# Optimization experiments

Measured on AMD Instinct MI355X. Metric: run time of the kernel, lower is better.

Reference implementation:

```python
import jax, jax.numpy as jnp
import numpy as np

B, S, D, H = 2, 2048, 1024, 16
DK = D // H

def setup_inputs() -> dict:
    key = jax.random.key(0)
    ks = jax.random.split(key, 8)
    inp = {
        "Q": jax.random.normal(ks[0], (B, S, D), dtype=jnp.float32),
        "K": jax.random.normal(ks[1], (B, S, D), dtype=jnp.float32),
        "V": jax.random.normal(ks[2], (B, S, D), dtype=jnp.float32),
        "mask": jax.random.randint(ks[3], (B, 1, S, S), 0, 2, dtype=jnp.int32),
        # nn.Linear weights, shape [out_features, in_features], no bias
        "Wq": jax.random.normal(ks[4], (D, D), dtype=jnp.float32) / np.sqrt(D),
        "Wk": jax.random.normal(ks[5], (D, D), dtype=jnp.float32) / np.sqrt(D),
        "Wv": jax.random.normal(ks[6], (D, D), dtype=jnp.float32) / np.sqrt(D),
        "Wo": jax.random.normal(ks[7], (D, D), dtype=jnp.float32) / np.sqrt(D),
    }
    return inp

def reference(Q, K, V, mask, Wq, Wk, Wv, Wo):
    b, s, d = Q.shape
    # projections: y = x @ W.T (torch nn.Linear convention)
    q = (Q @ Wq.T).reshape(b, s, H, DK).transpose(0, 2, 1, 3)  # [b,h,s,dk]
    k = (K @ Wk.T).reshape(b, -1, H, DK).transpose(0, 2, 1, 3)
    v = (V @ Wv.T).reshape(b, -1, H, DK).transpose(0, 2, 1, 3)
    score = jnp.einsum("bhqd,bhkd->bhqk", q, k) / jnp.sqrt(jnp.float32(DK))
    # faithful to source: masked positions get value 1e-9 BEFORE softmax
    score = jnp.where(mask == 0, jnp.float32(1e-9), score)
    attn = jax.nn.softmax(score, axis=-1)
    # dropout p=0.1 treated as eval-mode identity
    out = jnp.einsum("bhqk,bhkd->bhqd", attn, v)  # [b,h,s,dk]
    out = out.transpose(0, 2, 1, 3).reshape(b, s, d)
    return out @ Wo.T
```

## Files before the change

kernel.cpp:

```cpp
#include <hip/hip_runtime.h>

typedef unsigned short u16;
typedef __attribute__((ext_vector_type(8))) short bf16x8;
typedef __attribute__((ext_vector_type(4))) float f32x4;

constexpr int B_  = 2;
constexpr int S_  = 2048;
constexpr int D_  = 1024;
constexpr int H_  = 16;
constexpr int DK_ = 64;
constexpr int NROW = B_ * S_;
constexpr size_t QSZ  = (size_t)B_ * H_ * S_ * DK_;
constexpr size_t XBSZ = (size_t)NROW * D_;
constexpr size_t WBSZ = (size_t)D_ * D_;

__device__ __forceinline__ u16 f2bf(float f) {
    union { float f; unsigned u; } c; c.f = f;
    unsigned r = c.u + 0x7fffu + ((c.u >> 16) & 1u);
    return (u16)(r >> 16);
}
__device__ __forceinline__ unsigned pack2(float a, float b) {
    return (unsigned)f2bf(a) | ((unsigned)f2bf(b) << 16);
}

__device__ __forceinline__ void gl_lds16(const u16* g, u16* l) {
    __builtin_amdgcn_global_load_lds(
        (const __attribute__((address_space(1))) void*)g,
        (__attribute__((address_space(3))) void*)l, 16, 0, 0);
}

__global__ __launch_bounds__(256)
void cvt7(const float* __restrict__ s0, const float* __restrict__ s1,
          const float* __restrict__ s2, const float* __restrict__ s3,
          const float* __restrict__ s4, const float* __restrict__ s5,
          const float* __restrict__ s6,
          u16* __restrict__ d0, u16* __restrict__ d1, u16* __restrict__ d2,
          u16* __restrict__ d3, u16* __restrict__ d4, u16* __restrict__ d5,
          u16* __restrict__ d6)
{
    constexpr size_t XT = 3 * XBSZ;
    constexpr int NCHUNK = (int)((3 * XBSZ + 4 * WBSZ) / 2048);

    for (int c = blockIdx.x; c < NCHUNK; c += gridDim.x) {
        const size_t base = (size_t)c * 2048;
        const float* s; u16* d; size_t off;
        if (base < XT) {
            const int a = (int)(base >> 22);
            off = base & (XBSZ - 1);
            s = (a == 0) ? s0 : (a == 1) ? s1 : s2;
            d = (a == 0) ? d0 : (a == 1) ? d1 : d2;
        } else {
            const size_t r = base - XT;
            const int a = (int)(r >> 20);
            off = r & (WBSZ - 1);
            s = (a == 0) ? s3 : (a == 1) ? s4 : (a == 2) ? s5 : s6;
            d = (a == 0) ? d3 : (a == 1) ? d4 : (a == 2) ? d5 : d6;
        }
        const size_t e = off + (size_t)threadIdx.x * 8;
        const float4 x0 = *(const float4*)(s + e);
        const float4 x1 = *(const float4*)(s + e + 4);
        uint4 p;
        p.x = pack2(x0.x, x0.y); p.y = pack2(x0.z, x0.w);
        p.z = pack2(x1.x, x1.y); p.w = pack2(x1.z, x1.w);
        *(uint4*)(d + e) = p;
    }
}

__global__ __launch_bounds__(256, 3)
void qkv_gemm(const u16* __restrict__ Xq, const u16* __restrict__ Xk,
              const u16* __restrict__ Xv,
              const u16* __restrict__ Wq, const u16* __restrict__ Wk,
              const u16* __restrict__ Wv,
              u16* __restrict__ Yq, u16* __restrict__ Yk, u16* __restrict__ Yv)
{
    __shared__ u16 As[128 * 32];
    __shared__ u16 Bs[128 * 32];

    const int z = blockIdx.z;
    const u16* X = (z == 0) ? Xq : (z == 1) ? Xk : Xv;
    const u16* W = (z == 0) ? Wq : (z == 1) ? Wk : Wv;
    u16*       Y = (z == 0) ? Yq : (z == 1) ? Yk : Yv;
    const float osc = (z == 0) ? 0.125f : 1.0f;

    const int tid  = threadIdx.x;
    const int lane = tid & 63;
    const int w    = tid >> 6;
    const int quad = lane >> 4;
    const int lq   = lane & 15;
    const int wm   = (w & 1) << 6;
    const int wn   = (w >> 1) << 6;

    const int m0 = blockIdx.x << 7;
    const int n0 = blockIdx.y << 7;

    const int srow = tid >> 2;
    const int scol = (tid & 3) << 3;
    const u16* ga0 = X + (size_t)(m0 + srow) * D_ + scol;
    const u16* ga1 = ga0 + (size_t)64 * D_;
    const u16* gb0 = W + (size_t)(n0 + srow) * D_ + scol;
    const u16* gb1 = gb0 + (size_t)64 * D_;

    u16* la0 = As + (size_t)w * 512;
    u16* la1 = As + 2048 + (size_t)w * 512;
    u16* lb0 = Bs + (size_t)w * 512;
    u16* lb1 = Bs + 2048 + (size_t)w * 512;

    f32x4 acc[4][4];
#pragma unroll
    for (int i = 0; i < 4; ++i)
#pragma unroll
        for (int j = 0; j < 4; ++j) acc[i][j] = (f32x4){0.f, 0.f, 0.f, 0.f};

    for (int kt = 0; kt < D_; kt += 32) {
        __syncthreads();
        gl_lds16(ga0 + kt, la0);
        gl_lds16(ga1 + kt, la1);
        gl_lds16(gb0 + kt, lb0);
        gl_lds16(gb1 + kt, lb1);
        __syncthreads();

        bf16x8 af[4], bf[4];
#pragma unroll
        for (int t = 0; t < 4; ++t) {
            af[t] = *(const bf16x8*)&As[(size_t)(wm + (t << 4) + lq) * 32 + (quad << 3)];
            bf[t] = *(const bf16x8*)&Bs[(size_t)(wn + (t << 4) + lq) * 32 + (quad << 3)];
        }
#pragma unroll
        for (int i = 0; i < 4; ++i)
#pragma unroll
            for (int j = 0; j < 4; ++j)
                acc[i][j] = __builtin_amdgcn_mfma_f32_16x16x32_bf16(
                    af[i], bf[j], acc[i][j], 0, 0, 0);
    }

#pragma unroll
    for (int i = 0; i < 4; ++i)
#pragma unroll
        for (int j = 0; j < 4; ++j)
#pragma unroll
            for (int r = 0; r < 4; ++r) {
                const int grow = m0 + wm + (i << 4) + (quad << 2) + r;
                const int of   = n0 + wn + (j << 4) + lq;
                const int b = grow >> 11, s = grow & (S_ - 1);
                const int h = of >> 6,    dk = of & 63;
                Y[(((size_t)(b * H_ + h)) * S_ + s) * DK_ + dk] =
                    f2bf(acc[i][j][r] * osc);
            }
}

__global__ __launch_bounds__(256, 3)
void out_gemm(const u16* __restrict__ X, const u16* __restrict__ W,
              float* __restrict__ Y)
{
    __shared__ u16 As[128 * 32];
    __shared__ u16 Bs[128 * 32];

    const int tid  = threadIdx.x;
    const int lane = tid & 63;
    const int w    = tid >> 6;
    const int quad = lane >> 4;
    const int lq   = lane & 15;
    const int wm   = (w & 1) << 6;
    const int wn   = (w >> 1) << 6;

    const int m0 = blockIdx.x << 7;
    const int n0 = blockIdx.y << 7;

    const int srow = tid >> 2;
    const int scol = (tid & 3) << 3;
    const u16* ga0 = X + (size_t)(m0 + srow) * D_ + scol;
    const u16* ga1 = ga0 + (size_t)64 * D_;
    const u16* gb0 = W + (size_t)(n0 + srow) * D_ + scol;
    const u16* gb1 = gb0 + (size_t)64 * D_;

    u16* la0 = As + (size_t)w * 512;
    u16* la1 = As + 2048 + (size_t)w * 512;
    u16* lb0 = Bs + (size_t)w * 512;
    u16* lb1 = Bs + 2048 + (size_t)w * 512;

    f32x4 acc[4][4];
#pragma unroll
    for (int i = 0; i < 4; ++i)
#pragma unroll
        for (int j = 0; j < 4; ++j) acc[i][j] = (f32x4){0.f, 0.f, 0.f, 0.f};

    for (int kt = 0; kt < D_; kt += 32) {
        __syncthreads();
        gl_lds16(ga0 + kt, la0);
        gl_lds16(ga1 + kt, la1);
        gl_lds16(gb0 + kt, lb0);
        gl_lds16(gb1 + kt, lb1);
        __syncthreads();

        bf16x8 af[4], bf[4];
#pragma unroll
        for (int t = 0; t < 4; ++t) {
            af[t] = *(const bf16x8*)&As[(size_t)(wm + (t << 4) + lq) * 32 + (quad << 3)];
            bf[t] = *(const bf16x8*)&Bs[(size_t)(wn + (t << 4) + lq) * 32 + (quad << 3)];
        }
#pragma unroll
        for (int i = 0; i < 4; ++i)
#pragma unroll
            for (int j = 0; j < 4; ++j)
                acc[i][j] = __builtin_amdgcn_mfma_f32_16x16x32_bf16(
                    af[i], bf[j], acc[i][j], 0, 0, 0);
    }

#pragma unroll
    for (int i = 0; i < 4; ++i)
#pragma unroll
        for (int j = 0; j < 4; ++j)
#pragma unroll
            for (int r = 0; r < 4; ++r) {
                const int grow = m0 + wm + (i << 4) + (quad << 2) + r;
                const int gcol = n0 + wn + (j << 4) + lq;
                Y[(size_t)grow * D_ + gcol] = acc[i][j][r];
            }
}

constexpr int AP = 72;

__global__ __launch_bounds__(256, 2)
void attn_mfma4(const u16* __restrict__ qb, const u16* __restrict__ kb,
                const u16* __restrict__ vb, const int* __restrict__ mask,
                u16* __restrict__ ctx)
{
    __shared__ u16 Qs[128][AP];
    __shared__ u16 Ks[64][AP];
    __shared__ u16 Vt[64][AP];
    __shared__ u16 Ps[128][AP];

    const int tid  = threadIdx.x;
    const int lane = tid & 63;
    const int w    = tid >> 6;
    const int quad = lane >> 4;
    const int lq   = lane & 15;
    const int w32  = w << 5;

    const int q0 = blockIdx.x << 7;
    const int h  = blockIdx.y;
    const int b  = blockIdx.z;

    const u16* qbh = qb + (((size_t)b * H_ + h) * S_ + q0) * DK_;
    const u16* kbh = kb + ((size_t)b * H_ + h) * S_ * DK_;
    const u16* vbh = vb + ((size_t)b * H_ + h) * S_ * DK_;
    const int* mbh = mask + (size_t)b * S_ * S_;

    {
        const int r = tid >> 1, c = (tid & 1) << 5;
#pragma unroll
        for (int u = 0; u < 4; ++u)
            *(uint4*)&Qs[r][c + (u << 3)] =
                *(const uint4*)&qbh[(size_t)r * DK_ + c + (u << 3)];
    }
    __syncthreads();
    bf16x8 aQ[2][2];
#pragma unroll
    for (int i = 0; i < 2; ++i) {
        aQ[i][0] = *(const bf16x8*)&Qs[w32 + (i << 4) + lq][quad << 3];
        aQ[i][1] = *(const bf16x8*)&Qs[w32 + (i << 4) + lq][32 + (quad << 3)];
    }

    f32x4 O[2][4];
    float lsum[2][4];
#pragma unroll
    for (int i = 0; i < 2; ++i)
#pragma unroll
        for (int t = 0; t < 4; ++t) O[i][t] = (f32x4){0.f, 0.f, 0.f, 0.f};
#pragma unroll
    for (int i = 0; i < 2; ++i)
#pragma unroll
        for (int r = 0; r < 4; ++r) lsum[i][r] = 0.f;

    const int ksr = tid >> 2, ksc = (tid & 3) << 4;
    const int vkey = lane, vsc = w << 4;
    const int vpc  = ((vkey & 15) << 2) | (vkey >> 4);

    uint4 kr0, kr1; ushort4 vr[4];
    {
        kr0 = *(const uint4*)&kbh[(size_t)ksr * DK_ + ksc];
        kr1 = *(const uint4*)&kbh[(size_t)ksr * DK_ + ksc + 8];
#pragma unroll
        for (int u = 0; u < 4; ++u)
            vr[u] = *(const ushort4*)&vbh[(size_t)vkey * DK_ + vsc + (u << 2)];
    }

    const int qrow0 = q0 + w32 + (quad << 2);

    for (int k0 = 0; k0 < S_; k0 += 64) {
        int mreg[2][4][4];
#pragma unroll
        for (int i = 0; i < 2; ++i)
#pragma unroll
            for (int r = 0; r < 4; ++r)
#pragma unroll
                for (int t = 0; t < 4; ++t)
                    mreg[i][r][t] =
                        mbh[(size_t)(qrow0 + (i << 4) + r) * S_ + k0 + (t << 4) + lq];

        __syncthreads();
        {
            *(uint4*)&Ks[ksr][ksc]     = kr0;
            *(uint4*)&Ks[ksr][ksc + 8] = kr1;
            const u16 vv[16] = {
                vr[0].x, vr[0].y, vr[0].z, vr[0].w,
                vr[1].x, vr[1].y, vr[1].z, vr[1].w,
                vr[2].x, vr[2].y, vr[2].z, vr[2].w,
                vr[3].x, vr[3].y, vr[3].z, vr[3].w };
#pragma unroll
            for (int i = 0; i < 16; ++i)
                Vt[vsc + i][vpc] = vv[i];
        }
        __syncthreads();

        if (k0 + 64 < S_) {
            const size_t kb0 = (size_t)(k0 + 64 + ksr) * DK_ + ksc;
            kr0 = *(const uint4*)&kbh[kb0];
            kr1 = *(const uint4*)&kbh[kb0 + 8];
            const size_t vb0 = (size_t)(k0 + 64 + vkey) * DK_ + vsc;
#pragma unroll
            for (int u = 0; u < 4; ++u)
                vr[u] = *(const ushort4*)&vbh[vb0 + (u << 2)];
        }

        f32x4 st[2][4];
#pragma unroll
        for (int t = 0; t < 4; ++t) {
            const bf16x8 b0 = *(const bf16x8*)&Ks[(t << 4) + lq][quad << 3];
            const bf16x8 b1 = *(const bf16x8*)&Ks[(t << 4) + lq][32 + (quad << 3)];
#pragma unroll
            for (int i = 0; i < 2; ++i) {
                f32x4 c = {0.f, 0.f, 0.f, 0.f};
                c = __builtin_amdgcn_mfma_f32_16x16x32_bf16(aQ[i][0], b0, c, 0, 0, 0);
                c = __builtin_amdgcn_mfma_f32_16x16x32_bf16(aQ[i][1], b1, c, 0, 0, 0);
                st[i][t] = c;
            }
        }

#pragma unroll
        for (int i = 0; i < 2; ++i)
#pragma unroll
            for (int r = 0; r < 4; ++r) {
                float p0 = __expf(st[i][0][r]);
                float p1 = __expf(st[i][1][r]);
                float p2 = __expf(st[i][2][r]);
                float p3 = __expf(st[i][3][r]);
                p0 = (mreg[i][r][0] == 0) ? 1.0f : p0;
                p1 = (mreg[i][r][1] == 0) ? 1.0f : p1;
                p2 = (mreg[i][r][2] == 0) ? 1.0f : p2;
                p3 = (mreg[i][r][3] == 0) ? 1.0f : p3;
                lsum[i][r] += (p0 + p1) + (p2 + p3);
                ushort4 pk;
                pk.x = f2bf(p0); pk.y = f2bf(p1);
                pk.z = f2bf(p2); pk.w = f2bf(p3);
                *(ushort4*)&Ps[w32 + (i << 4) + (quad << 2) + r][lq << 2] = pk;
            }

        bf16x8 aP[2][2];
#pragma unroll
        for (int i = 0; i < 2; ++i) {
            aP[i][0] = *(const bf16x8*)&Ps[w32 + (i << 4) + lq][quad << 3];
            aP[i][1] = *(const bf16x8*)&Ps[w32 + (i << 4) + lq][32 + (quad << 3)];
        }
#pragma unroll
        for (int t = 0; t < 4; ++t) {
            const bf16x8 b0 = *(const bf16x8*)&Vt[(t << 4) + lq][quad << 3];
            const bf16x8 b1 = *(const bf16x8*)&Vt[(t << 4) + lq][32 + (quad << 3)];
#pragma unroll
            for (int i = 0; i < 2; ++i) {
                O[i][t] = __builtin_amdgcn_mfma_f32_16x16x32_bf16(aP[i][0], b0, O[i][t], 0, 0, 0);
                O[i][t] = __builtin_amdgcn_mfma_f32_16x16x32_bf16(aP[i][1], b1, O[i][t], 0, 0, 0);
            }
        }
    }

#pragma unroll
    for (int i = 0; i < 2; ++i)
#pragma unroll
        for (int r = 0; r < 4; ++r) {
#pragma unroll
            for (int off = 1; off < 16; off <<= 1)
                lsum[i][r] += __shfl_xor(lsum[i][r], off);
            lsum[i][r] = 1.0f / lsum[i][r];
        }

#pragma unroll
    for (int i = 0; i < 2; ++i)
#pragma unroll
        for (int t = 0; t < 4; ++t)
#pragma unroll
            for (int r = 0; r < 4; ++r) {
                const int row = qrow0 + (i << 4) + r;
                ctx[((size_t)b * S_ + row) * D_ + (h << 6) + (t << 4) + lq] =
                    f2bf(O[i][t][r] * lsum[i][r]);
            }
}

extern "C" void kernel_launch(void* const* d_in, const int* in_sizes, int n_in,
                              void* d_out, int out_size, void* d_ws, size_t ws_size,
                              hipStream_t stream)
{
    const float* Q    = (const float*)d_in[0];
    const float* K    = (const float*)d_in[1];
    const float* V    = (const float*)d_in[2];
    const int*   mask = (const int*)d_in[3];
    const float* Wq   = (const float*)d_in[4];
    const float* Wk   = (const float*)d_in[5];
    const float* Wv   = (const float*)d_in[6];
    const float* Wo   = (const float*)d_in[7];
    float* out = (float*)d_out;

    u16* xqb = (u16*)d_ws;
    u16* xkb = xqb + XBSZ;
    u16* xvb = xqb + 2 * XBSZ;
    u16* wqb = xqb + 3 * XBSZ;
    u16* wkb = wqb + WBSZ;
    u16* wvb = wqb + 2 * WBSZ;
    u16* wob = wqb + 3 * WBSZ;
    u16* qw  = wqb + 4 * WBSZ;
    u16* kw  = qw + QSZ;
    u16* vw  = qw + 2 * QSZ;
    u16* cx  = xqb;

    const dim3 blk(256);

    hipLaunchKernelGGL(cvt7, dim3(2048), blk, 0, stream,
                       Q, K, V, Wq, Wk, Wv, Wo,
                       xqb, xkb, xvb, wqb, wkb, wvb, wob);
    hipLaunchKernelGGL(qkv_gemm, dim3(NROW / 128, D_ / 128, 3), blk, 0, stream,
                       xqb, xkb, xvb, wqb, wkb, wvb, qw, kw, vw);
    hipLaunchKernelGGL(attn_mfma4, dim3(S_ / 128, H_, B_), blk, 0, stream,
                       qw, kw, vw, mask, cx);
    hipLaunchKernelGGL(out_gemm, dim3(NROW / 128, D_ / 128), blk, 0, stream,
                       cx, wob, out);
}
```

Before: 257.0 us.

## Bit-pack the attention mask once and read packed bits in attention

The conversion kernel now also compresses the int32 mask into a one-bit-per-entry array, and the attention kernel reads 64-bit words of mask bits per row instead of 16 int32 loads per row per tile. Each head previously reread the full int32 mask, so this targets the large repeated mask traffic across 16 heads. The bf16 packing of probabilities also switches to the hardware v_cvt_pk_bf16_f32 instruction. In exchange there is an extra pass over the 32 MB mask in the pre-kernel plus extra workspace, and the mask bit selection costs a few ALU ops per element.

```diff
diff --git a/kernel.cpp b/kernel.cpp
--- a/kernel.cpp
+++ b/kernel.cpp
@@ -1,6 +1,8 @@
 #include <hip/hip_runtime.h>
 
 typedef unsigned short u16;
+typedef unsigned char  u8;
+typedef unsigned long long u64;
 typedef __attribute__((ext_vector_type(8))) short bf16x8;
 typedef __attribute__((ext_vector_type(4))) float f32x4;
 
@@ -13,6 +15,8 @@
 constexpr size_t QSZ  = (size_t)B_ * H_ * S_ * DK_;
 constexpr size_t XBSZ = (size_t)NROW * D_;
 constexpr size_t WBSZ = (size_t)D_ * D_;
+constexpr size_t MSZ  = (size_t)B_ * S_ * S_;
+constexpr size_t MPKB = MSZ / 8;
 
 __device__ __forceinline__ u16 f2bf(float f) {
     union { float f; unsigned u; } c; c.f = f;
@@ -22,6 +26,11 @@
 __device__ __forceinline__ unsigned pack2(float a, float b) {
     return (unsigned)f2bf(a) | ((unsigned)f2bf(b) << 16);
 }
+__device__ __forceinline__ unsigned cvt_pk_bf16(float a, float b) {
+    unsigned r;
+    asm("v_cvt_pk_bf16_f32 %0, %1, %2" : "=v"(r) : "v"(a), "v"(b));
+    return r;
+}
 
 __device__ __forceinline__ void gl_lds16(const u16* g, u16* l) {
     __builtin_amdgcn_global_load_lds(
@@ -30,39 +39,51 @@
 }
 
 __global__ __launch_bounds__(256)
-void cvt7(const float* __restrict__ s0, const float* __restrict__ s1,
-          const float* __restrict__ s2, const float* __restrict__ s3,
-          const float* __restrict__ s4, const float* __restrict__ s5,
-          const float* __restrict__ s6,
-          u16* __restrict__ d0, u16* __restrict__ d1, u16* __restrict__ d2,
-          u16* __restrict__ d3, u16* __restrict__ d4, u16* __restrict__ d5,
-          u16* __restrict__ d6)
+void cvt7m(const float* __restrict__ s0, const float* __restrict__ s1,
+           const float* __restrict__ s2, const float* __restrict__ s3,
+           const float* __restrict__ s4, const float* __restrict__ s5,
+           const float* __restrict__ s6, const int* __restrict__ mk,
+           u16* __restrict__ d0, u16* __restrict__ d1, u16* __restrict__ d2,
+           u16* __restrict__ d3, u16* __restrict__ d4, u16* __restrict__ d5,
+           u16* __restrict__ d6, u8* __restrict__ mp)
 {
     constexpr size_t XT = 3 * XBSZ;
-    constexpr int NCHUNK = (int)((3 * XBSZ + 4 * WBSZ) / 2048);
-
-    for (int c = blockIdx.x; c < NCHUNK; c += gridDim.x) {
-        const size_t base = (size_t)c * 2048;
-        const float* s; u16* d; size_t off;
-        if (base < XT) {
-            const int a = (int)(base >> 22);
-            off = base & (XBSZ - 1);
-            s = (a == 0) ? s0 : (a == 1) ? s1 : s2;
-            d = (a == 0) ? d0 : (a == 1) ? d1 : d2;
+    constexpr int NCF = (int)((3 * XBSZ + 4 * WBSZ) / 2048);
+    constexpr int NCM = (int)(MSZ / 2048);
+
+    for (int c = blockIdx.x; c < NCF + NCM; c += gridDim.x) {
+        if (c < NCF) {
+            const size_t base = (size_t)c * 2048;
+            const float* s; u16* d; size_t off;
+            if (base < XT) {
+                const int a = (int)(base >> 22);
+                off = base & (XBSZ - 1);
+                s = (a == 0) ? s0 : (a == 1) ? s1 : s2;
+                d = (a == 0) ? d0 : (a == 1) ? d1 : d2;
+            } else {
+                const size_t r = base - XT;
+                const int a = (int)(r >> 20);
+                off = r & (WBSZ - 1);
+                s = (a == 0) ? s3 : (a == 1) ? s4 : (a == 2) ? s5 : s6;
+                d = (a == 0) ? d3 : (a == 1) ? d4 : (a == 2) ? d5 : d6;
+            }
+            const size_t e = off + (size_t)threadIdx.x * 8;
+            const float4 x0 = *(const float4*)(s + e);
+            const float4 x1 = *(const float4*)(s + e + 4);
+            uint4 p;
+            p.x = pack2(x0.x, x0.y); p.y = pack2(x0.z, x0.w);
+            p.z = pack2(x1.x, x1.y); p.w = pack2(x1.z, x1.w);
+            *(uint4*)(d + e) = p;
         } else {
-            const size_t r = base - XT;
-            const int a = (int)(r >> 20);
-            off = r & (WBSZ - 1);
-            s = (a == 0) ? s3 : (a == 1) ? s4 : (a == 2) ? s5 : s6;
-            d = (a == 0) ? d3 : (a == 1) ? d4 : (a == 2) ? d5 : d6;
-        }
-        const size_t e = off + (size_t)threadIdx.x * 8;
-        const float4 x0 = *(const float4*)(s + e);
-        const float4 x1 = *(const float4*)(s + e + 4);
-        uint4 p;
-        p.x = pack2(x0.x, x0.y); p.y = pack2(x0.z, x0.w);
-        p.z = pack2(x1.x, x1.y); p.w = pack2(x1.z, x1.w);
-        *(uint4*)(d + e) = p;
+            const size_t e = (size_t)(c - NCF) * 2048 + (size_t)threadIdx.x * 8;
+            const int4 x0 = *(const int4*)(mk + e);
+            const int4 x1 = *(const int4*)(mk + e + 4);
+            unsigned bv = (unsigned)(x0.x != 0)        | ((unsigned)(x0.y != 0) << 1)
+                        | ((unsigned)(x0.z != 0) << 2) | ((unsigned)(x0.w != 0) << 3)
+                        | ((unsigned)(x1.x != 0) << 4) | ((unsigned)(x1.y != 0) << 5)
+                        | ((unsigned)(x1.z != 0) << 6) | ((unsigned)(x1.w != 0) << 7);
+            mp[e >> 3] = (u8)bv;
+        }
     }
 }
 
@@ -221,8 +242,8 @@
 constexpr int AP = 72;
 
 __global__ __launch_bounds__(256, 2)
-void attn_mfma4(const u16* __restrict__ qb, const u16* __restrict__ kb,
-                const u16* __restrict__ vb, const int* __restrict__ mask,
+void attn_mfma5(const u16* __restrict__ qb, const u16* __restrict__ kb,
+                const u16* __restrict__ vb, const u8* __restrict__ mpk,
                 u16* __restrict__ ctx)
 {
     __shared__ u16 Qs[128][AP];
@@ -244,7 +265,7 @@
     const u16* qbh = qb + (((size_t)b * H_ + h) * S_ + q0) * DK_;
     const u16* kbh = kb + ((size_t)b * H_ + h) * S_ * DK_;
     const u16* vbh = vb + ((size_t)b * H_ + h) * S_ * DK_;
-    const int* mbh = mask + (size_t)b * S_ * S_;
+    const u8*  mbh = mpk + (size_t)b * S_ * (S_ / 8);
 
     {
         const int r = tid >> 1, c = (tid & 1) << 5;
@@ -286,17 +307,15 @@
     }
 
     const int qrow0 = q0 + w32 + (quad << 2);
+    const u8* mrow = mbh + (size_t)qrow0 * (S_ / 8);
 
     for (int k0 = 0; k0 < S_; k0 += 64) {
-        int mreg[2][4][4];
+        u64 mw[2][4];
 #pragma unroll
         for (int i = 0; i < 2; ++i)
 #pragma unroll
             for (int r = 0; r < 4; ++r)
-#pragma unroll
-                for (int t = 0; t < 4; ++t)
-                    mreg[i][r][t] =
-                        mbh[(size_t)(qrow0 + (i << 4) + r) * S_ + k0 + (t << 4) + lq];
+                mw[i][r] = *(const u64*)&mrow[(size_t)((i << 4) + r) * (S_ / 8) + (k0 >> 3)];
 
         __syncthreads();
         {
@@ -341,19 +360,21 @@
         for (int i = 0; i < 2; ++i)
 #pragma unroll
             for (int r = 0; r < 4; ++r) {
+                const unsigned lo = (unsigned)mw[i][r];
+                const unsigned hi = (unsigned)(mw[i][r] >> 32);
                 float p0 = __expf(st[i][0][r]);
                 float p1 = __expf(st[i][1][r]);
                 float p2 = __expf(st[i][2][r]);
                 float p3 = __expf(st[i][3][r]);
-                p0 = (mreg[i][r][0] == 0) ? 1.0f : p0;
-                p1 = (mreg[i][r][1] == 0) ? 1.0f : p1;
-                p2 = (mreg[i][r][2] == 0) ? 1.0f : p2;
-                p3 = (mreg[i][r][3] == 0) ? 1.0f : p3;
+                p0 = ((lo >> lq) & 1u) ? p0 : 1.0f;
+                p1 = ((lo >> (lq + 16)) & 1u) ? p1 : 1.0f;
+                p2 = ((hi >> lq) & 1u) ? p2 : 1.0f;
+                p3 = ((hi >> (lq + 16)) & 1u) ? p3 : 1.0f;
                 lsum[i][r] += (p0 + p1) + (p2 + p3);
-                ushort4 pk;
-                pk.x = f2bf(p0); pk.y = f2bf(p1);
-                pk.z = f2bf(p2); pk.w = f2bf(p3);
-                *(ushort4*)&Ps[w32 + (i << 4) + (quad << 2) + r][lq << 2] = pk;
+                uint2 pw;
+                pw.x = cvt_pk_bf16(p0, p1);
+                pw.y = cvt_pk_bf16(p2, p3);
+                *(uint2*)&Ps[w32 + (i << 4) + (quad << 2) + r][lq << 2] = pw;
             }
 
         bf16x8 aP[2][2];
@@ -420,17 +441,18 @@
     u16* qw  = wqb + 4 * WBSZ;
     u16* kw  = qw + QSZ;
     u16* vw  = qw + 2 * QSZ;
+    u8*  mpk = (u8*)(qw + 3 * QSZ);
     u16* cx  = xqb;
 
     const dim3 blk(256);
 
-    hipLaunchKernelGGL(cvt7, dim3(2048), blk, 0, stream,
-                       Q, K, V, Wq, Wk, Wv, Wo,
-                       xqb, xkb, xvb, wqb, wkb, wvb, wob);
+    hipLaunchKernelGGL(cvt7m, dim3(2048), blk, 0, stream,
+                       Q, K, V, Wq, Wk, Wv, Wo, mask,
+                       xqb, xkb, xvb, wqb, wkb, wvb, wob, mpk);
     hipLaunchKernelGGL(qkv_gemm, dim3(NROW / 128, D_ / 128, 3), blk, 0, stream,
                        xqb, xkb, xvb, wqb, wkb, wvb, qw, kw, vw);
-    hipLaunchKernelGGL(attn_mfma4, dim3(S_ / 128, H_, B_), blk, 0, stream,
-                       qw, kw, vw, mask, cx);
+    hipLaunchKernelGGL(attn_mfma5, dim3(S_ / 128, H_, B_), blk, 0, stream,
+                       qw, kw, vw, mpk, cx);
     hipLaunchKernelGGL(out_gemm, dim3(NROW / 128, D_ / 128), blk, 0, stream,
                        cx, wob, out);
 }
```

Result: no change. 254.8 us (-0.9%).
